# Performance work log

Measured on AMD Instinct MI355X. Metric: run time of the kernel, lower is better.

## Reference

```python
import jax, jax.numpy as jnp
import numpy as np

N_NODES = 50000
N_EDGES = 600000
D_IN = 128
D_OUT = 128
LN_EPS = 1e-5


def setup_inputs() -> dict:
    key = jax.random.key(0)
    ks = jax.random.split(key, 12)
    x = jax.random.normal(ks[0], (N_NODES, D_IN), dtype=jnp.float32)
    adj_in_rows = jax.random.randint(ks[1], (N_EDGES,), 0, N_NODES, dtype=jnp.int32)
    adj_in_cols = jax.random.randint(ks[2], (N_EDGES,), 0, N_NODES, dtype=jnp.int32)
    adj_in_vals = jax.random.uniform(ks[3], (N_EDGES,), dtype=jnp.float32)
    adj_out_rows = jax.random.randint(ks[4], (N_EDGES,), 0, N_NODES, dtype=jnp.int32)
    adj_out_cols = jax.random.randint(ks[5], (N_EDGES,), 0, N_NODES, dtype=jnp.int32)
    adj_out_vals = jax.random.uniform(ks[6], (N_EDGES,), dtype=jnp.float32)
    s = 1.0 / np.sqrt(D_IN)
    W_self = jax.random.uniform(ks[7], (D_OUT, D_IN), dtype=jnp.float32, minval=-s, maxval=s)
    b_self = jax.random.uniform(ks[8], (D_OUT,), dtype=jnp.float32, minval=-s, maxval=s)
    W_in = jax.random.uniform(ks[9], (D_OUT, D_IN), dtype=jnp.float32, minval=-s, maxval=s)
    W_out = jax.random.uniform(ks[10], (D_OUT, D_IN), dtype=jnp.float32, minval=-s, maxval=s)
    ln_gamma = jnp.ones((D_OUT,), dtype=jnp.float32)
    ln_beta = jnp.zeros((D_OUT,), dtype=jnp.float32)
    return {
        "x": x,
        "adj_in_rows": adj_in_rows, "adj_in_cols": adj_in_cols, "adj_in_vals": adj_in_vals,
        "adj_out_rows": adj_out_rows, "adj_out_cols": adj_out_cols, "adj_out_vals": adj_out_vals,
        "W_self": W_self, "b_self": b_self, "W_in": W_in, "W_out": W_out,
        "ln_gamma": ln_gamma, "ln_beta": ln_beta,
    }


def _spmm(rows, cols, vals, x, n):
    # COO sparse.mm: out[r] += vals[e] * x[cols[e]]
    return jax.ops.segment_sum(vals[:, None] * x[cols], rows, num_segments=n)


def reference(x, adj_in_rows, adj_in_cols, adj_in_vals,
              adj_out_rows, adj_out_cols, adj_out_vals,
              W_self, b_self, W_in, W_out, ln_gamma, ln_beta):
    n = x.shape[0]
    agg_in = _spmm(adj_in_rows, adj_in_cols, adj_in_vals, x, n)
    agg_out = _spmm(adj_out_rows, adj_out_cols, adj_out_vals, x, n)
    h = x @ W_self.T + b_self + agg_in @ W_in.T + agg_out @ W_out.T
    mu = jnp.mean(h, axis=-1, keepdims=True)
    var = jnp.mean(jnp.square(h - mu), axis=-1, keepdims=True)
    h = (h - mu) * jax.lax.rsqrt(var + LN_EPS) * ln_gamma + ln_beta
    # dropout is identity in eval mode (training=False)
    return jax.nn.relu(h)
```

## Files before the change

### kernel.cpp

```cpp
#include <hip/hip_runtime.h>

#define N_NODES 50000
#define N_EDGES 600000
#define D 128
#define BM 32
#define NT (2 * N_NODES)
#define NE2 (2 * N_EDGES)
#define NPAD 50048
#define KA 384
#define GBM 64
#define NBB 1563
#define CAPB 2048
#define CHUNK_A 4096

typedef __attribute__((ext_vector_type(8))) short bf16x8;
typedef __attribute__((ext_vector_type(4))) float f32x4;

__device__ inline unsigned short bfr(float x) {
    unsigned b = __float_as_uint(x);
    b += 0x7FFFu + ((b >> 16) & 1u);
    return (unsigned short)(b >> 16);
}
__device__ inline float bf_lo(unsigned u) { return __uint_as_float(u << 16); }
__device__ inline float bf_hi(unsigned u) { return __uint_as_float(u & 0xFFFF0000u); }

#define G1 (NPAD * 32 / 256)
#define G2 192
#define NZI (NBB + 48 * 128)
#define G3 ((NZI + 255) / 256)

__global__ __launch_bounds__(256) void prep(
    const float* __restrict__ x, const float* __restrict__ Ws,
    const float* __restrict__ Wi, const float* __restrict__ Wo,
    short* __restrict__ A, short* __restrict__ Wc, int* __restrict__ bcnt)
{
    const int bid = blockIdx.x, t = threadIdx.x;
    if (bid < G1) {
        int gid = bid * 256 + t;
        int row = gid >> 5, c4 = gid & 31;
        ushort4 o = {0, 0, 0, 0};
        if (row < N_NODES) {
            float4 v = *reinterpret_cast<const float4*>(x + (size_t)row * D + c4 * 4);
            o.x = bfr(v.x); o.y = bfr(v.y); o.z = bfr(v.z); o.w = bfr(v.w);
        }
        *reinterpret_cast<ushort4*>(A + (size_t)row * KA + c4 * 4) = o;
    } else if (bid < G1 + G2) {
        int gid = (bid - G1) * 256 + t;
        int j = gid / 384, k = gid - j * 384;
        float v = (k < 128) ? Ws[j * 128 + k]
                : (k < 256) ? Wi[j * 128 + k - 128]
                            : Wo[j * 128 + k - 256];
        Wc[j * KA + k] = (short)bfr(v);
    } else {
        int z = (bid - G1 - G2) * 256 + t;
        if (z < NBB) bcnt[z] = 0;
        else if (z < NZI) {
            int z2 = z - NBB;
            int row = N_NODES + (z2 >> 7);
            int o = z2 & 127;
            ((int*)A)[(size_t)row * (KA / 2) + 64 + o] = 0;
        }
    }
}


__global__ __launch_bounds__(1024) void bucket_hist(
    const int* __restrict__ ir, const int* __restrict__ orow, int* __restrict__ bcnt)
{
    __shared__ int h[NBB];
    for (int i = threadIdx.x; i < NBB; i += 1024) h[i] = 0;
    __syncthreads();
    int stride = gridDim.x * 1024;
    for (int e = blockIdx.x * 1024 + threadIdx.x; e < NE2; e += stride) {
        int rid = (e < N_EDGES) ? ir[e] : N_NODES + orow[e - N_EDGES];
        atomicAdd(&h[rid >> 6], 1);
    }
    __syncthreads();
    for (int i = threadIdx.x; i < NBB; i += 1024)
        if (h[i]) atomicAdd(&bcnt[i], h[i]);
}

__global__ __launch_bounds__(1024) void scan_buckets(
    const int* __restrict__ bcnt, int* __restrict__ bbase, int* __restrict__ bcur)
{
    __shared__ int s[1024];
    const int t = threadIdx.x;
    const int i0 = 2 * t, i1 = 2 * t + 1;
    int v0 = (i0 < NBB) ? bcnt[i0] : 0;
    int v1 = (i1 < NBB) ? bcnt[i1] : 0;
    int v = v0 + v1;
    s[t] = v;
    __syncthreads();
    for (int o = 1; o < 1024; o <<= 1) {
        int u = (t >= o) ? s[t - o] : 0;
        __syncthreads();
        s[t] += u;
        __syncthreads();
    }
    int ex = s[t] - v;
    if (i0 < NBB) { bbase[i0] = ex;      bcur[i0] = ex; }
    if (i1 < NBB) { bbase[i1] = ex + v0; bcur[i1] = ex + v0; }
}

__global__ __launch_bounds__(1024) void scatter_chunks(
    const int* __restrict__ ir, const int* __restrict__ icol, const float* __restrict__ ival,
    const int* __restrict__ orow, const int* __restrict__ ocol, const float* __restrict__ oval,
    int* __restrict__ bcur, int2* __restrict__ pairp)
{
    __shared__ int2 pay[CHUNK_A];
    __shared__ int  dstp[CHUNK_A];
    __shared__ int  hist[NBB];
    __shared__ int  gb2[NBB];
    __shared__ int  sbuf[1024];

    const int t = threadIdx.x;
    for (int i = t; i < NBB; i += 1024) hist[i] = 0;
    __syncthreads();

    const int e0 = blockIdx.x * CHUNK_A;
    const int m = min(NE2 - e0, CHUNK_A);
    int bk4[4], px4[4], vv4[4];
#pragma unroll
    for (int i = 0; i < 4; ++i) {
        int e = e0 + t + i * 1024;
        int rid, col; float val;
        if (e < N_EDGES)      { rid = ir[e];                       col = icol[e];            val = ival[e]; }
        else if (e < NE2)     { rid = N_NODES + orow[e - N_EDGES]; col = ocol[e - N_EDGES];  val = oval[e - N_EDGES]; }
        else                  { rid = -1; col = 0; val = 0.f; }
        if (rid >= 0) {
            bk4[i] = rid >> 6;
            px4[i] = (col & 0xFFFF) | ((rid & 63) << 16);
            vv4[i] = __float_as_int(val);
            atomicAdd(&hist[bk4[i]], 1);
        } else bk4[i] = -1;
    }
    __syncthreads();

    const int i0 = 2 * t, i1 = 2 * t + 1;
    int v0 = (i0 < NBB) ? hist[i0] : 0;
    int v1 = (i1 < NBB) ? hist[i1] : 0;
    int v = v0 + v1;
    sbuf[t] = v;
    __syncthreads();
    for (int o = 1; o < 1024; o <<= 1) {
        int u = (t >= o) ? sbuf[t - o] : 0;
        __syncthreads();
        sbuf[t] += u;
        __syncthreads();
    }
    int ex = sbuf[t] - v;
    if (i0 < NBB) {
        int g = v0 ? atomicAdd(&bcur[i0], v0) : 0;
        gb2[i0] = g - ex;
        hist[i0] = ex;
    }
    if (i1 < NBB) {
        int g = v1 ? atomicAdd(&bcur[i1], v1) : 0;
        gb2[i1] = g - (ex + v0);
        hist[i1] = ex + v0;
    }
    __syncthreads();

#pragma unroll
    for (int i = 0; i < 4; ++i) {
        if (bk4[i] < 0) continue;
        int s = atomicAdd(&hist[bk4[i]], 1);
        pay[s]  = make_int2(px4[i], vv4[i]);
        dstp[s] = gb2[bk4[i]] + s;
    }
    __syncthreads();

    for (int i = t; i < m; i += 1024)
        pairp[dstp[i]] = pay[i];
}

__global__ __launch_bounds__(256) void row_sort(
    const int* __restrict__ bbase, const int* __restrict__ bcnt,
    const int2* __restrict__ pairp, int2* __restrict__ pairp2,
    int* __restrict__ row_ptr)
{
    __shared__ int2 pay[CAPB];
    __shared__ int  rs[64];
    __shared__ int  rcur[64];

    const int b = blockIdx.x, t = threadIdx.x;
    const int base = bbase[b];
    const int n = bcnt[b];

    if (t < 64) rs[t] = 0;
    __syncthreads();

    const bool fast = (n <= CAPB);
    if (fast) {
        for (int i = t; i < n; i += 256) {
            int2 p = pairp[base + i];
            pay[i] = p;
            atomicAdd(&rs[(p.x >> 16) & 63], 1);
        }
    } else {
        for (int i = t; i < n; i += 256)
            atomicAdd(&rs[(pairp[base + i].x >> 16) & 63], 1);
    }
    __syncthreads();

    if (t < 64) {
        int v = rs[t];
        int a = v;
#pragma unroll
        for (int o = 1; o < 64; o <<= 1) {
            int u = __shfl_up(a, o);
            if (t >= o) a += u;
        }
        int ex = a - v;
        rcur[t] = ex;
        row_ptr[b * 64 + t] = base + ex;
    }
    __syncthreads();

    if (fast) {
        for (int i = t; i < n; i += 256) {
            int2 p = pay[i];
            int pos = atomicAdd(&rcur[(p.x >> 16) & 63], 1);
            pairp2[base + pos] = p;
        }
    } else {
        for (int i = t; i < n; i += 256) {
            int2 p = pairp[base + i];
            int pos = atomicAdd(&rcur[(p.x >> 16) & 63], 1);
            pairp2[base + pos] = p;
        }
    }
}

__global__ __launch_bounds__(256) void gather_rows(
    const int* __restrict__ row_ptr, const int2* __restrict__ pairp2,
    short* __restrict__ A)
{
    const int wv = blockIdx.x * 4 + (threadIdx.x >> 6);
    if (wv >= NT) return;
    const int lane = threadIdx.x & 63;
    int s = row_ptr[wv];
    int e = row_ptr[wv + 1];
    s = __builtin_amdgcn_readfirstlane(s);
    e = __builtin_amdgcn_readfirstlane(e);

    const char* Ab = (const char*)A + lane * 4;
    float ax = 0.f, ay = 0.f;

    for (int i = s; i < e; i += 8) {
#pragma unroll
        for (int k = 0; k < 8; ++k) {
            int idx = i + k;
            int2 p = pairp2[min(idx, e - 1)];
            float v = (idx < e) ? __int_as_float(p.y) : 0.f;
            unsigned u = *(const unsigned*)(Ab + (unsigned)((p.x & 0xFFFF) * (KA * 2)));
            ax += v * bf_lo(u);
            ay += v * bf_hi(u);
        }
    }

    unsigned o = ((unsigned)bfr(ay) << 16) | (unsigned)bfr(ax);
    size_t dst = (wv < N_NODES)
               ? ((size_t)wv * (KA * 2) + 256 + lane * 4)
               : ((size_t)(wv - N_NODES) * (KA * 2) + 512 + lane * 4);
    *(unsigned*)((char*)A + dst) = o;
}

__global__ __launch_bounds__(512) void gemm_mfma(
    const short* __restrict__ A, const short* __restrict__ Wc,
    const float* __restrict__ b, const float* __restrict__ gamma,
    const float* __restrict__ beta, float* __restrict__ out)
{
    __shared__ short Alds[GBM * KA];
    __shared__ float red[8][64][2];
    __shared__ float2 mustd[64];

    const int t = threadIdx.x;
    const int l = t & 63, w = t >> 6;
    const int q = l >> 4, c = l & 15;
    const int base = blockIdx.x * GBM;

    bf16x8 bfrag[12];
    const short* wrow = Wc + (size_t)(w * 16 + c) * KA + q * 8;
#pragma unroll
    for (int s = 0; s < 12; ++s)
        bfrag[s] = *reinterpret_cast<const bf16x8*>(wrow + s * 32);

#pragma unroll
    for (int i = 0; i < 6; ++i) {
        int slot = t + i * 512;
        int row = slot / 48, c16 = slot % 48;
        bf16x8 v = *reinterpret_cast<const bf16x8*>(A + (size_t)(base + row) * KA + c16 * 8);
        *reinterpret_cast<bf16x8*>(&Alds[row * KA + (c16 ^ (row & 7)) * 8]) = v;
    }
    __syncthreads();

    f32x4 acc[4];
#pragma unroll
    for (int rg = 0; rg < 4; ++rg) acc[rg] = (f32x4){0.f, 0.f, 0.f, 0.f};

#pragma unroll
    for (int s = 0; s < 12; ++s) {
#pragma unroll
        for (int rg = 0; rg < 4; ++rg) {
            int row = rg * 16 + c;
            int c16 = (s * 4 + q) ^ (row & 7);
            bf16x8 af = *reinterpret_cast<const bf16x8*>(&Alds[row * KA + c16 * 8]);
            acc[rg] = __builtin_amdgcn_mfma_f32_16x16x32_bf16(af, bfrag[s], acc[rg], 0, 0, 0);
        }
    }

    const float bj = b[w * 16 + c];
    const float gj = gamma[w * 16 + c];
    const float ej = beta[w * 16 + c];

#pragma unroll
    for (int rg = 0; rg < 4; ++rg) {
#pragma unroll
        for (int r = 0; r < 4; ++r) {
            float hv = acc[rg][r] + bj;
            acc[rg][r] = hv;
            float s1 = hv, s2 = hv * hv;
#pragma unroll
            for (int m = 1; m < 16; m <<= 1) {
                s1 += __shfl_xor(s1, m);
                s2 += __shfl_xor(s2, m);
            }
            if (c == 0) {
                int row = rg * 16 + q * 4 + r;
                red[w][row][0] = s1;
                red[w][row][1] = s2;
            }
        }
    }
    __syncthreads();

    if (t < 64) {
        float s1 = 0.f, s2 = 0.f;
#pragma unroll
        for (int ww = 0; ww < 8; ++ww) { s1 += red[ww][t][0]; s2 += red[ww][t][1]; }
        float mu = s1 * (1.f / 128.f);
        float var = s2 * (1.f / 128.f) - mu * mu;
        mustd[t] = make_float2(mu, rsqrtf(var + 1e-5f));
    }
    __syncthreads();

#pragma unroll
    for (int rg = 0; rg < 4; ++rg) {
        int row0 = rg * 16 + q * 4;
        int node0 = base + row0;
#pragma unroll
        for (int r = 0; r < 4; ++r) {
            float2 ms = mustd[row0 + r];
            float y = (acc[rg][r] - ms.x) * ms.y * gj + ej;
            y = fmaxf(y, 0.f);
            if (node0 + r < N_NODES)
                out[(size_t)(node0 + r) * D + w * 16 + c] = y;
        }
    }
}

__global__ __launch_bounds__(256) void spmm_scatter(
    const int* __restrict__ rows, const int* __restrict__ cols,
    const float* __restrict__ vals, const float* __restrict__ x,
    float* __restrict__ agg, int nE)
{
    int g = blockIdx.x * 256 + threadIdx.x;
    int e = g >> 5;
    if (e >= nE) return;
    int q = g & 31;
    int r = rows[e], c = cols[e];
    float v = vals[e];
    float4 xv = *reinterpret_cast<const float4*>(x + (size_t)c * D + (size_t)q * 4);
    float* ap = agg + (size_t)r * D + (size_t)q * 4;
    atomicAdd(ap + 0, v * xv.x);
    atomicAdd(ap + 1, v * xv.y);
    atomicAdd(ap + 2, v * xv.z);
    atomicAdd(ap + 3, v * xv.w);
}

__global__ __launch_bounds__(256) void gemm_ln_relu(
    const float* __restrict__ x, const float* __restrict__ agg_in,
    const float* __restrict__ agg_out,
    const float* __restrict__ Ws, const float* __restrict__ Wi,
    const float* __restrict__ Wo, const float* __restrict__ b,
    const float* __restrict__ gamma, const float* __restrict__ beta,
    float* __restrict__ out, int n)
{
    __shared__ float4 Wl[D * (D / 4)];
    __shared__ float4 Xl[BM * (D / 4)];

    const int t = threadIdx.x;
    const int l = t & 63;
    const int w = t >> 6;
    const int base = blockIdx.x * BM;
    const int j0 = l, j1 = l + 64;

    float acc0[8], acc1[8];
    const float bj0 = b[j0], bj1 = b[j1];
#pragma unroll
    for (int i = 0; i < 8; ++i) { acc0[i] = bj0; acc1[i] = bj1; }

    const float* srcs[3] = { x, agg_in, agg_out };
    const float* wms[3]  = { Ws, Wi, Wo };

#pragma unroll
    for (int s = 0; s < 3; ++s) {
        const float4* src4 = reinterpret_cast<const float4*>(srcs[s]);
        const float4* w4   = reinterpret_cast<const float4*>(wms[s]);
        __syncthreads();
#pragma unroll
        for (int it = 0; it < 16; ++it) {
            int gi = t + 256 * it;
            int j = gi >> 5, k4 = gi & 31;
            Wl[j * 32 + (k4 ^ (j & 7))] = w4[gi];
        }
#pragma unroll
        for (int it = 0; it < 4; ++it) {
            int gi = t + 256 * it;
            int m = gi >> 5, k4 = gi & 31;
            int node = base + m;
            float4 v = (node < n) ? src4[(size_t)node * 32 + k4]
                                  : make_float4(0.f, 0.f, 0.f, 0.f);
            Xl[m * 32 + k4] = v;
        }
        __syncthreads();

        const int sw = j0 & 7;
#pragma unroll 8
        for (int k4 = 0; k4 < 32; ++k4) {
            float4 w0 = Wl[j0 * 32 + (k4 ^ sw)];
            float4 w1 = Wl[j1 * 32 + (k4 ^ sw)];
#pragma unroll
            for (int i = 0; i < 8; ++i) {
                float4 xv = Xl[(w + 4 * i) * 32 + k4];
                acc0[i] += xv.x * w0.x + xv.y * w0.y + xv.z * w0.z + xv.w * w0.w;
                acc1[i] += xv.x * w1.x + xv.y * w1.y + xv.z * w1.z + xv.w * w1.w;
            }
        }
    }

    const float g0 = gamma[j0], g1 = gamma[j1];
    const float be0 = beta[j0], be1 = beta[j1];
#pragma unroll
    for (int i = 0; i < 8; ++i) {
        int node = base + w + 4 * i;
        float s  = acc0[i] + acc1[i];
        float ss = acc0[i] * acc0[i] + acc1[i] * acc1[i];
#pragma unroll
        for (int off = 32; off; off >>= 1) {
            s  += __shfl_xor(s, off);
            ss += __shfl_xor(ss, off);
        }
        float mu   = s * (1.0f / D);
        float var  = ss * (1.0f / D) - mu * mu;
        float rstd = rsqrtf(var + 1e-5f);
        if (node < n) {
            float y0 = (acc0[i] - mu) * rstd * g0 + be0;
            float y1 = (acc1[i] - mu) * rstd * g1 + be1;
            out[(size_t)node * D + j0] = fmaxf(y0, 0.f);
            out[(size_t)node * D + j1] = fmaxf(y1, 0.f);
        }
    }
}

extern "C" void kernel_launch(void* const* d_in, const int* in_sizes, int n_in,
                              void* d_out, int out_size, void* d_ws, size_t ws_size,
                              hipStream_t stream) {
    const float* x     = (const float*)d_in[0];
    const int*   ir    = (const int*)  d_in[1];
    const int*   icoln = (const int*)  d_in[2];
    const float* ival  = (const float*)d_in[3];
    const int*   orow  = (const int*)  d_in[4];
    const int*   ocol  = (const int*)  d_in[5];
    const float* oval  = (const float*)d_in[6];
    const float* Ws    = (const float*)d_in[7];
    const float* b     = (const float*)d_in[8];
    const float* Wi    = (const float*)d_in[9];
    const float* Wo    = (const float*)d_in[10];
    const float* gamma = (const float*)d_in[11];
    const float* beta  = (const float*)d_in[12];
    float* out = (float*)d_out;

    short* A       = (short*)d_ws;
    short* Wc      = A + (size_t)NPAD * KA;
    int*   bcnt    = (int*)(Wc + (size_t)128 * KA);
    int*   bbase   = bcnt + NBB;
    int*   bcur    = bbase + NBB;
    int*   row_ptr = bcur + NBB;
    uintptr_t pp   = (uintptr_t)(row_ptr + NBB * 64 + 1);
    pp = (pp + 7) & ~(uintptr_t)7;
    int2*  pairp   = (int2*)pp;
    int2*  pairp2  = pairp + NE2;
    size_t need    = (size_t)((char*)(pairp2 + NE2) - (char*)d_ws);

    if (ws_size >= need) {
        prep<<<G1 + G2 + G3, 256, 0, stream>>>(x, Ws, Wi, Wo, A, Wc, bcnt);
        bucket_hist<<<128, 1024, 0, stream>>>(ir, orow, bcnt);
        scan_buckets<<<1, 1024, 0, stream>>>(bcnt, bbase, bcur);
        scatter_chunks<<<(NE2 + CHUNK_A - 1) / CHUNK_A, 1024, 0, stream>>>(
            ir, icoln, ival, orow, ocol, oval, bcur, pairp);
        row_sort<<<NBB, 256, 0, stream>>>(bbase, bcnt, pairp, pairp2, row_ptr);
        gather_rows<<<(NT + 3) / 4, 256, 0, stream>>>(row_ptr, pairp2, A);
        gemm_mfma<<<NPAD / GBM, 512, 0, stream>>>(A, Wc, b, gamma, beta, out);
    } else {
        float* agg_in  = (float*)d_ws;
        float* agg_out = agg_in + (size_t)N_NODES * D;
        hipMemsetAsync(d_ws, 0, 2 * (size_t)N_NODES * D * sizeof(float), stream);
        const int eblocks = (N_EDGES * 32 + 255) / 256;
        spmm_scatter<<<eblocks, 256, 0, stream>>>(ir, icoln, ival, x, agg_in, N_EDGES);
        spmm_scatter<<<eblocks, 256, 0, stream>>>(orow, ocol, oval, x, agg_out, N_EDGES);
        const int gblocks = (N_NODES + BM - 1) / BM;
        gemm_ln_relu<<<gblocks, 256, 0, stream>>>(x, agg_in, agg_out, Ws, Wi, Wo,
                                                  b, gamma, beta, out, N_NODES);
    }
}
```

Baseline: 128.4 us.

## Fuse bucket histogram into prep kernel and make row gather persistent

```diff
diff --git a/kernel.cpp b/kernel.cpp
--- a/kernel.cpp
+++ b/kernel.cpp
@@ -12,6 +12,7 @@
 #define NBB 1563
 #define CAPB 2048
 #define CHUNK_A 4096
+#define GW 8192
 
 typedef __attribute__((ext_vector_type(8))) short bf16x8;
 typedef __attribute__((ext_vector_type(4))) float f32x4;
@@ -26,14 +27,17 @@
 
 #define G1 (NPAD * 32 / 256)
 #define G2 192
-#define NZI (NBB + 48 * 128)
+#define NZI (48 * 128)
 #define G3 ((NZI + 255) / 256)
+#define G4 256
 
 __global__ __launch_bounds__(256) void prep(
     const float* __restrict__ x, const float* __restrict__ Ws,
     const float* __restrict__ Wi, const float* __restrict__ Wo,
+    const int* __restrict__ ir, const int* __restrict__ orow,
     short* __restrict__ A, short* __restrict__ Wc, int* __restrict__ bcnt)
 {
+    __shared__ int h[NBB];
     const int bid = blockIdx.x, t = threadIdx.x;
     if (bid < G1) {
         int gid = bid * 256 + t;
@@ -51,33 +55,25 @@
                 : (k < 256) ? Wi[j * 128 + k - 128]
                             : Wo[j * 128 + k - 256];
         Wc[j * KA + k] = (short)bfr(v);
+    } else if (bid < G1 + G2 + G3) {
+        int z = (bid - G1 - G2) * 256 + t;
+        if (z < NZI) {
+            int row = N_NODES + (z >> 7);
+            int o = z & 127;
+            ((int*)A)[(size_t)row * (KA / 2) + 64 + o] = 0;
+        }
     } else {
-        int z = (bid - G1 - G2) * 256 + t;
-        if (z < NBB) bcnt[z] = 0;
-        else if (z < NZI) {
-            int z2 = z - NBB;
-            int row = N_NODES + (z2 >> 7);
-            int o = z2 & 127;
-            ((int*)A)[(size_t)row * (KA / 2) + 64 + o] = 0;
-        }
-    }
-}
-
-
-__global__ __launch_bounds__(1024) void bucket_hist(
-    const int* __restrict__ ir, const int* __restrict__ orow, int* __restrict__ bcnt)
-{
-    __shared__ int h[NBB];
-    for (int i = threadIdx.x; i < NBB; i += 1024) h[i] = 0;
-    __syncthreads();
-    int stride = gridDim.x * 1024;
-    for (int e = blockIdx.x * 1024 + threadIdx.x; e < NE2; e += stride) {
-        int rid = (e < N_EDGES) ? ir[e] : N_NODES + orow[e - N_EDGES];
-        atomicAdd(&h[rid >> 6], 1);
-    }
-    __syncthreads();
-    for (int i = threadIdx.x; i < NBB; i += 1024)
-        if (h[i]) atomicAdd(&bcnt[i], h[i]);
+        for (int i = t; i < NBB; i += 256) h[i] = 0;
+        __syncthreads();
+        int bb = bid - (G1 + G2 + G3);
+        for (int e = bb * 256 + t; e < NE2; e += G4 * 256) {
+            int rid = (e < N_EDGES) ? ir[e] : N_NODES + orow[e - N_EDGES];
+            atomicAdd(&h[rid >> 6], 1);
+        }
+        __syncthreads();
+        for (int i = t; i < NBB; i += 256)
+            if (h[i]) atomicAdd(&bcnt[i], h[i]);
+    }
 }
 
 __global__ __launch_bounds__(1024) void scan_buckets(
@@ -236,34 +232,35 @@
     const int* __restrict__ row_ptr, const int2* __restrict__ pairp2,
     short* __restrict__ A)
 {
-    const int wv = blockIdx.x * 4 + (threadIdx.x >> 6);
-    if (wv >= NT) return;
+    const int wid = blockIdx.x * 4 + (threadIdx.x >> 6);
     const int lane = threadIdx.x & 63;
-    int s = row_ptr[wv];
-    int e = row_ptr[wv + 1];
-    s = __builtin_amdgcn_readfirstlane(s);
-    e = __builtin_amdgcn_readfirstlane(e);
-
     const char* Ab = (const char*)A + lane * 4;
-    float ax = 0.f, ay = 0.f;
-
-    for (int i = s; i < e; i += 8) {
-#pragma unroll
-        for (int k = 0; k < 8; ++k) {
-            int idx = i + k;
-            int2 p = pairp2[min(idx, e - 1)];
-            float v = (idx < e) ? __int_as_float(p.y) : 0.f;
-            unsigned u = *(const unsigned*)(Ab + (unsigned)((p.x & 0xFFFF) * (KA * 2)));
-            ax += v * bf_lo(u);
-            ay += v * bf_hi(u);
-        }
-    }
-
-    unsigned o = ((unsigned)bfr(ay) << 16) | (unsigned)bfr(ax);
-    size_t dst = (wv < N_NODES)
-               ? ((size_t)wv * (KA * 2) + 256 + lane * 4)
-               : ((size_t)(wv - N_NODES) * (KA * 2) + 512 + lane * 4);
-    *(unsigned*)((char*)A + dst) = o;
+
+    for (int wv = wid; wv < NT; wv += GW) {
+        int s = row_ptr[wv];
+        int e = row_ptr[wv + 1];
+        s = __builtin_amdgcn_readfirstlane(s);
+        e = __builtin_amdgcn_readfirstlane(e);
+
+        float ax = 0.f, ay = 0.f;
+        for (int i = s; i < e; i += 16) {
+#pragma unroll
+            for (int k = 0; k < 16; ++k) {
+                int idx = i + k;
+                int2 p = pairp2[min(idx, e - 1)];
+                float v = (idx < e) ? __int_as_float(p.y) : 0.f;
+                unsigned u = *(const unsigned*)(Ab + (unsigned)((p.x & 0xFFFF) * (KA * 2)));
+                ax += v * bf_lo(u);
+                ay += v * bf_hi(u);
+            }
+        }
+
+        unsigned o = ((unsigned)bfr(ay) << 16) | (unsigned)bfr(ax);
+        size_t dst = (wv < N_NODES)
+                   ? ((size_t)wv * (KA * 2) + 256 + lane * 4)
+                   : ((size_t)(wv - N_NODES) * (KA * 2) + 512 + lane * 4);
+        *(unsigned*)((char*)A + dst) = o;
+    }
 }
 
 __global__ __launch_bounds__(512) void gemm_mfma(
@@ -495,13 +492,13 @@
     size_t need    = (size_t)((char*)(pairp2 + NE2) - (char*)d_ws);
 
     if (ws_size >= need) {
-        prep<<<G1 + G2 + G3, 256, 0, stream>>>(x, Ws, Wi, Wo, A, Wc, bcnt);
-        bucket_hist<<<128, 1024, 0, stream>>>(ir, orow, bcnt);
+        hipMemsetAsync(bcnt, 0, NBB * sizeof(int), stream);
+        prep<<<G1 + G2 + G3 + G4, 256, 0, stream>>>(x, Ws, Wi, Wo, ir, orow, A, Wc, bcnt);
         scan_buckets<<<1, 1024, 0, stream>>>(bcnt, bbase, bcur);
         scatter_chunks<<<(NE2 + CHUNK_A - 1) / CHUNK_A, 1024, 0, stream>>>(
             ir, icoln, ival, orow, ocol, oval, bcur, pairp);
         row_sort<<<NBB, 256, 0, stream>>>(bbase, bcnt, pairp, pairp2, row_ptr);
-        gather_rows<<<(NT + 3) / 4, 256, 0, stream>>>(row_ptr, pairp2, A);
+        gather_rows<<<GW / 4, 256, 0, stream>>>(row_ptr, pairp2, A);
         gemm_mfma<<<NPAD / GBM, 512, 0, stream>>>(A, Wc, b, gamma, beta, out);
     } else {
         float* agg_in  = (float*)d_ws;
```

Result: slower. 143.2 us (+11.5%).
